# Performance work log

Measured on AMD Instinct MI355X. Metric: run time of the kernel, lower is better.

Reference implementation:

```python
import jax, jax.numpy as jnp
import numpy as np

DIM = 1024

def setup_inputs() -> dict:
    key = jax.random.key(0)
    ks = jax.random.split(key, 6)
    B, T, D = 8, 2048, DIM
    s = 1.0 / np.sqrt(D)
    x = jax.random.normal(ks[0], (B, T, D), dtype=jnp.float32)
    Wq = jax.random.normal(ks[1], (D, D), dtype=jnp.float32) * s
    Wk = jax.random.normal(ks[2], (D, D), dtype=jnp.float32) * s
    Wv = jax.random.normal(ks[3], (D, D), dtype=jnp.float32) * s
    Wp = jax.random.normal(ks[4], (D, D), dtype=jnp.float32) * s
    bp = jax.random.normal(ks[5], (D,), dtype=jnp.float32) * 0.01
    return {"x": x, "Wq": Wq, "Wk": Wk, "Wv": Wv, "Wp": Wp, "bp": bp}

def reference(x, Wq, Wk, Wv, Wp, bp):
    # x: [b, t, d]; weights stored as [d_in, d_out] (torch Linear applies x @ W.T;
    # here we bake the transpose into the stored matrix).
    scale = x.shape[-1] ** (-0.5)
    q = jnp.einsum('btd,de->bte', x, Wq)
    k = jnp.einsum('btd,de->bte', x, Wk)
    v = jnp.einsum('btd,de->bte', x, Wv)
    attn = jax.nn.softmax(jnp.einsum('btd,bTd->btT', q, k) * scale, axis=-1)
    out = jnp.einsum('btT,bTd->btd', attn, v)
    return jnp.einsum('btd,de->bte', out, Wp) + bp
```

## Files before the change

kernel.cpp:

```cpp
#include <hip/hip_runtime.h>


typedef _Float16 half_t;
typedef _Float16 half8 __attribute__((ext_vector_type(8)));
typedef float floatx4 __attribute__((ext_vector_type(4)));

#define GLD16(gp, lp)                                                          \
    __builtin_amdgcn_global_load_lds(                                          \
        (const __attribute__((address_space(1))) void*)(gp),                   \
        (__attribute__((address_space(3))) void*)(lp), 16, 0, 0)

#define WAIT_VM0()  asm volatile("s_waitcnt vmcnt(0)" ::: "memory")
#define BARRIER()   do { asm volatile("" ::: "memory");                        \
                         __builtin_amdgcn_s_barrier();                         \
                         asm volatile("" ::: "memory"); } while (0)

template<int EPI>
__global__ __launch_bounds__(512, 4)
void gemm16(const half_t* __restrict__ A, const half_t* __restrict__ B,
            void* __restrict__ Cv, void* __restrict__ C2, void* __restrict__ C3,
            const float* __restrict__ bias, int K, int lda, int ldb, int ldc,
            long long bsA, long long bsB, long long bsC)
{
    __shared__ half_t As[2 * 256 * 32];
    __shared__ half_t Bs[2 * 128 * 32];

    const int tid  = threadIdx.x;
    const int lane = tid & 63;
    const int wid  = tid >> 6;
    const int wr   = (wid >> 1) * 64;
    const int wc   = (wid & 1) * 64;
    const long long z = blockIdx.z;
    const int rowBase = blockIdx.y * 256;
    const int colBase = blockIdx.x * 128;

    const int lrow = lane >> 2;
    const int scol = (((lane & 3) ^ ((lane >> 3) & 3))) * 8;

    const half_t* gptr[3];
    int  lofs[3];
    bool isA[3];
    #pragma unroll
    for (int j = 0; j < 3; ++j) {
        const int r16 = (wid * 3 + j) * 16;
        if (r16 < 256) {
            gptr[j] = A + z * bsA + (long long)(rowBase + r16 + lrow) * lda + scol;
            lofs[j] = r16 * 32;
            isA[j]  = true;
        } else {
            gptr[j] = B + z * bsB + (long long)(colBase + (r16 - 256) + lrow) * ldb + scol;
            lofs[j] = (r16 - 256) * 32;
            isA[j]  = false;
        }
    }

    floatx4 acc[4][4];
    #pragma unroll
    for (int m = 0; m < 4; ++m)
        #pragma unroll
        for (int n = 0; n < 4; ++n)
            #pragma unroll
            for (int j = 0; j < 4; ++j) acc[m][n][j] = 0.0f;

    const int fr  = lane & 15;
    const int fks = (((lane >> 4) ^ ((lane >> 1) & 3))) * 8;
    const int nIter = K >> 5;

    #pragma unroll
    for (int j = 0; j < 3; ++j)
        GLD16(gptr[j], isA[j] ? &As[lofs[j]] : &Bs[lofs[j]]);
    WAIT_VM0();
    BARRIER();

    for (int it = 0; it < nIter; ++it) {
        const int ca = (it & 1) * 8192;
        const int cb = (it & 1) * 4096;
        const int na = 8192 - ca;
        const int nb = 4096 - cb;
        if (it + 1 < nIter) {
            const int kk = (it + 1) << 5;
            #pragma unroll
            for (int j = 0; j < 3; ++j)
                GLD16(gptr[j] + kk, isA[j] ? &As[na + lofs[j]] : &Bs[nb + lofs[j]]);
        }

        half8 af[4], bf[4];
        #pragma unroll
        for (int m = 0; m < 4; ++m)
            af[m] = *(const half8*)&As[ca + (wr + m * 16 + fr) * 32 + fks];
        #pragma unroll
        for (int n = 0; n < 4; ++n)
            bf[n] = *(const half8*)&Bs[cb + (wc + n * 16 + fr) * 32 + fks];
        #pragma unroll
        for (int m = 0; m < 4; ++m)
            #pragma unroll
            for (int n = 0; n < 4; ++n)
                acc[m][n] = __builtin_amdgcn_mfma_f32_16x16x32_f16(af[m], bf[n], acc[m][n], 0, 0, 0);

        WAIT_VM0();
        BARRIER();
    }

    const int ecol = lane & 15;
    const int q4   = (lane >> 4) * 4;
    #pragma unroll
    for (int m = 0; m < 4; ++m) {
        #pragma unroll
        for (int n = 0; n < 4; ++n) {
            const int gcol = colBase + wc + n * 16 + ecol;
            #pragma unroll
            for (int r = 0; r < 4; ++r) {
                const int grow = rowBase + wr + m * 16 + q4 + r;
                float v = acc[m][n][r];
                if (EPI == 0) {
                    ((half_t*)Cv)[z * bsC + (long long)grow * ldc + gcol] = (half_t)v;
                } else if (EPI == 1) {
                    ((float*)Cv)[(long long)grow * ldc + gcol] = v + bias[gcol];
                } else {
                    const int mat = colBase >> 10;
                    const int c   = gcol & 1023;
                    if (mat == 0) {
                        ((half_t*)Cv)[(long long)grow * 1024 + c] = (half_t)(v * 0.03125f);
                    } else if (mat == 1) {
                        ((half_t*)C2)[(long long)grow * 1024 + c] = (half_t)v;
                    } else {
                        const long long bb = grow >> 11;
                        const long long tt = grow & 2047;
                        ((half_t*)C3)[bb * (1024LL * 2048) + (long long)c * 2048 + tt] = (half_t)v;
                    }
                }
            }
        }
    }
}

__global__ __launch_bounds__(256)
void cast16(const float* __restrict__ x, half_t* __restrict__ y)
{
    const long long i = ((long long)blockIdx.x * 256 + threadIdx.x) * 8;
    floatx4 a = *(const floatx4*)(x + i);
    floatx4 b = *(const floatx4*)(x + i + 4);
    half8 h;
    #pragma unroll
    for (int j = 0; j < 4; ++j) { h[j] = (half_t)a[j]; h[j + 4] = (half_t)b[j]; }
    *(half8*)(y + i) = h;
}

__global__ __launch_bounds__(256)
void cast_transpose4(const float* __restrict__ W0, const float* __restrict__ W1,
                     const float* __restrict__ W2, const float* __restrict__ W3,
                     half_t* __restrict__ WT)
{
    const float* W = (blockIdx.z == 0) ? W0 : (blockIdx.z == 1) ? W1
                   : (blockIdx.z == 2) ? W2 : W3;
    half_t* O = WT + (long long)blockIdx.z * 1024 * 1024;
    __shared__ float t[32][33];
    const int bx = blockIdx.x * 32, by = blockIdx.y * 32;
    const int tx = threadIdx.x, ty = threadIdx.y;
    #pragma unroll
    for (int i = 0; i < 32; i += 8)
        t[ty + i][tx] = W[(long long)(by + ty + i) * 1024 + bx + tx];
    __syncthreads();
    #pragma unroll
    for (int i = 0; i < 32; i += 8)
        O[(long long)(bx + ty + i) * 1024 + by + tx] = (half_t)t[tx][ty + i];
}

__global__ __launch_bounds__(256)
void softmax_rows(half_t* __restrict__ S)
{
    const long long base = (long long)blockIdx.x * 2048;
    const int t = threadIdx.x;
    half8 h = *(const half8*)(S + base + t * 8);
    float v[8];
    #pragma unroll
    for (int i = 0; i < 8; ++i) v[i] = (float)h[i];
    float m = -3.0e38f;
    #pragma unroll
    for (int i = 0; i < 8; ++i) m = fmaxf(m, v[i]);
    #pragma unroll
    for (int off = 32; off > 0; off >>= 1) m = fmaxf(m, __shfl_down(m, off));
    __shared__ float redm[4], reds[4];
    const int lane = t & 63, wid = t >> 6;
    if (lane == 0) redm[wid] = m;
    __syncthreads();
    const float M = fmaxf(fmaxf(redm[0], redm[1]), fmaxf(redm[2], redm[3]));
    float s = 0.f;
    #pragma unroll
    for (int i = 0; i < 8; ++i) { v[i] = __expf(v[i] - M); s += v[i]; }
    #pragma unroll
    for (int off = 32; off > 0; off >>= 1) s += __shfl_down(s, off);
    if (lane == 0) reds[wid] = s;
    __syncthreads();
    const float inv = 1.0f / (reds[0] + reds[1] + reds[2] + reds[3]);
    #pragma unroll
    for (int i = 0; i < 8; ++i) h[i] = (half_t)(v[i] * inv);
    *(half8*)(S + base + t * 8) = h;
}

extern "C" void kernel_launch(void* const* d_in, const int* in_sizes, int n_in,
                              void* d_out, int out_size, void* d_ws, size_t ws_size,
                              hipStream_t stream)
{
    const float* x  = (const float*)d_in[0];
    const float* Wq = (const float*)d_in[1];
    const float* Wk = (const float*)d_in[2];
    const float* Wv = (const float*)d_in[3];
    const float* Wp = (const float*)d_in[4];
    const float* bp = (const float*)d_in[5];
    float* out = (float*)d_out;

    char* ws = (char*)d_ws;
    const long long MB = 1024LL * 1024LL;
    half_t* WqkvT = (half_t*)(ws + 0 * MB);
    half_t* WpT   = (half_t*)(ws + 6 * MB);
    half_t* q     = (half_t*)(ws + 8 * MB);
    half_t* k     = (half_t*)(ws + 40 * MB);
    half_t* vT    = (half_t*)(ws + 72 * MB);
    half_t* x16   = (half_t*)(ws + 104 * MB);
    half_t* S     = (half_t*)(ws + 104 * MB);

    dim3 blk(512);
    cast16<<<8192, dim3(256), 0, stream>>>(x, x16);
    cast_transpose4<<<dim3(32, 32, 4), dim3(32, 8), 0, stream>>>(Wq, Wk, Wv, Wp, WqkvT);

    gemm16<2><<<dim3(24, 64, 1), blk, 0, stream>>>(
        x16, WqkvT, q, k, vT, nullptr, 1024, 1024, 1024, 0, 0, 0, 0);

    gemm16<0><<<dim3(16, 8, 8), blk, 0, stream>>>(
        q, k, S, nullptr, nullptr, nullptr, 1024, 1024, 1024, 2048,
        2048LL * 1024, 2048LL * 1024, 2048LL * 2048);

    softmax_rows<<<8 * 2048, dim3(256), 0, stream>>>(S);

    gemm16<0><<<dim3(8, 8, 8), blk, 0, stream>>>(
        S, vT, q, nullptr, nullptr, nullptr, 2048, 2048, 2048, 1024,
        2048LL * 2048, 1024LL * 2048, 2048LL * 1024);

    gemm16<1><<<dim3(8, 64, 1), blk, 0, stream>>>(
        q, WpT, out, nullptr, nullptr, bp, 1024, 1024, 1024, 1024, 0, 0, 0);
}
```

Measured before the change: 542.7 us.

## Rework GEMM to 256x256x64 tiles with phased LDS loads and XCD-aware block remap

Raises the GEMM block tile from 256x128x32 to 256x256x64, with each of 8 waves computing a 128x64 sub-tile. Loads are staged in phases with lgkmcnt waits, barriers and s_setprio around the MFMA bursts. It also remaps block IDs so neighbouring tiles land on the same XCD, which should improve L2 reuse. The aim is higher arithmetic intensity per LDS/global byte and fewer K-loop iterations, at the cost of more registers (launch bounds drop to 2 blocks per CU), more LDS, and half as many blocks in each launch.

```diff
diff --git a/kernel.cpp b/kernel.cpp
--- a/kernel.cpp
+++ b/kernel.cpp
@@ -10,107 +10,156 @@
         (const __attribute__((address_space(1))) void*)(gp),                   \
         (__attribute__((address_space(3))) void*)(lp), 16, 0, 0)
 
-#define WAIT_VM0()  asm volatile("s_waitcnt vmcnt(0)" ::: "memory")
+#define WAIT_VM0()   asm volatile("s_waitcnt vmcnt(0)" ::: "memory")
+#define WAIT_LGKM0() asm volatile("s_waitcnt lgkmcnt(0)" ::: "memory")
+#define WAIT_LGKM8() asm volatile("s_waitcnt lgkmcnt(8)" ::: "memory")
 #define BARRIER()   do { asm volatile("" ::: "memory");                        \
                          __builtin_amdgcn_s_barrier();                         \
                          asm volatile("" ::: "memory"); } while (0)
 
 template<int EPI>
-__global__ __launch_bounds__(512, 4)
+__global__ __launch_bounds__(512, 2)
 void gemm16(const half_t* __restrict__ A, const half_t* __restrict__ B,
             void* __restrict__ Cv, void* __restrict__ C2, void* __restrict__ C3,
             const float* __restrict__ bias, int K, int lda, int ldb, int ldc,
             long long bsA, long long bsB, long long bsC)
 {
-    __shared__ half_t As[2 * 256 * 32];
-    __shared__ half_t Bs[2 * 128 * 32];
+    __shared__ half_t As[2 * 2 * 128 * 64];
+    __shared__ half_t Bs[2 * 2 * 128 * 64];
 
     const int tid  = threadIdx.x;
     const int lane = tid & 63;
-    const int wid  = tid >> 6;
-    const int wr   = (wid >> 1) * 64;
-    const int wc   = (wid & 1) * 64;
-    const long long z = blockIdx.z;
-    const int rowBase = blockIdx.y * 256;
-    const int colBase = blockIdx.x * 128;
-
-    const int lrow = lane >> 2;
-    const int scol = (((lane & 3) ^ ((lane >> 3) & 3))) * 8;
-
-    const half_t* gptr[3];
-    int  lofs[3];
-    bool isA[3];
-    #pragma unroll
-    for (int j = 0; j < 3; ++j) {
-        const int r16 = (wid * 3 + j) * 16;
-        if (r16 < 256) {
-            gptr[j] = A + z * bsA + (long long)(rowBase + r16 + lrow) * lda + scol;
-            lofs[j] = r16 * 32;
-            isA[j]  = true;
-        } else {
-            gptr[j] = B + z * bsB + (long long)(colBase + (r16 - 256) + lrow) * ldb + scol;
-            lofs[j] = (r16 - 256) * 32;
-            isA[j]  = false;
-        }
-    }
-
-    floatx4 acc[4][4];
-    #pragma unroll
-    for (int m = 0; m < 4; ++m)
+    const int w    = tid >> 6;
+    const int wm   = w >> 2;
+    const int wn   = w & 3;
+
+    int bx = blockIdx.x, by = blockIdx.y, bz = blockIdx.z;
+    {
+        const int gx = gridDim.x, gy = gridDim.y;
+        const int nwg = gx * gy * (int)gridDim.z;
+        int lid = (bz * gy + by) * gx + bx;
+        const int qq = nwg >> 3, rr = nwg & 7;
+        const int xcd = lid & 7, off = lid >> 3;
+        lid = (xcd < rr ? xcd * (qq + 1) : rr * (qq + 1) + (xcd - rr) * qq) + off;
+        bx = lid % gx; lid /= gx;
+        by = lid % gy; bz = lid / gy;
+    }
+    const long long z = bz;
+    const int rowBase = by * 256;
+    const int colBase = bx * 256;
+
+    const int srow = lane >> 3;
+    const int schk = (lane & 7) ^ srow;
+    const half_t* gp[4];
+    int jstep[4];
+    half_t* lp[4];
+    #pragma unroll
+    for (int i = 0; i < 4; ++i) {
+        const bool ia = (i < 2);
+        const int ld  = ia ? lda : ldb;
+        const int rb  = (ia ? rowBase : colBase) + (i & 1) * 128 + w * 16 + srow;
+        gp[i] = (ia ? A + z * bsA : B + z * bsB) + (long long)rb * ld + schk * 8;
+        jstep[i] = 8 * ld;
+        lp[i] = (ia ? As : Bs) + (i & 1) * 8192 + w * 1024;
+    }
+
+    const int fr  = lane & 15;
+    const int q   = lane >> 4;
+    const int rsw = fr & 7;
+    const half_t* Abase = As + wm * 8192 + fr * 64;
+    const half_t* Bbase = Bs + (wn >> 1) * 8192 + ((wn & 1) * 64 + fr) * 64;
+    const int ko0 = ((0 + q) ^ rsw) * 8;
+    const int ko1 = ((4 + q) ^ rsw) * 8;
+
+    floatx4 acc[8][4];
+    #pragma unroll
+    for (int m = 0; m < 8; ++m)
         #pragma unroll
         for (int n = 0; n < 4; ++n)
             #pragma unroll
             for (int j = 0; j < 4; ++j) acc[m][n][j] = 0.0f;
 
-    const int fr  = lane & 15;
-    const int fks = (((lane >> 4) ^ ((lane >> 1) & 3))) * 8;
-    const int nIter = K >> 5;
-
-    #pragma unroll
-    for (int j = 0; j < 3; ++j)
-        GLD16(gptr[j], isA[j] ? &As[lofs[j]] : &Bs[lofs[j]]);
+    const int nIter = K >> 6;
+
+    #pragma unroll
+    for (int i = 0; i < 4; ++i) {
+        GLD16(gp[i],            lp[i]);
+        GLD16(gp[i] + jstep[i], lp[i] + 512);
+    }
     WAIT_VM0();
     BARRIER();
 
-    for (int it = 0; it < nIter; ++it) {
-        const int ca = (it & 1) * 8192;
-        const int cb = (it & 1) * 4096;
-        const int na = 8192 - ca;
-        const int nb = 4096 - cb;
-        if (it + 1 < nIter) {
-            const int kk = (it + 1) << 5;
-            #pragma unroll
-            for (int j = 0; j < 3; ++j)
-                GLD16(gptr[j] + kk, isA[j] ? &As[na + lofs[j]] : &Bs[nb + lofs[j]]);
-        }
-
-        half8 af[4], bf[4];
-        #pragma unroll
-        for (int m = 0; m < 4; ++m)
-            af[m] = *(const half8*)&As[ca + (wr + m * 16 + fr) * 32 + fks];
-        #pragma unroll
-        for (int n = 0; n < 4; ++n)
-            bf[n] = *(const half8*)&Bs[cb + (wc + n * 16 + fr) * 32 + fks];
-        #pragma unroll
-        for (int m = 0; m < 4; ++m)
+    for (int t = 0; t < nIter; ++t) {
+        const int cbuf = (t & 1) << 14;
+        const int nbuf = 16384 - cbuf;
+        half8 bf[4][2], af[2][2];
+
+        if (t + 1 < nIter) {
+            const int kk = (t + 1) << 6;
+            #pragma unroll
+            for (int i = 0; i < 4; ++i) {
+                GLD16(gp[i] + kk,            lp[i] + nbuf);
+                GLD16(gp[i] + kk + jstep[i], lp[i] + nbuf + 512);
+            }
+        }
+        #pragma unroll
+        for (int n = 0; n < 4; ++n) {
+            bf[n][0] = *(const half8*)(Bbase + cbuf + n * 1024 + ko0);
+            bf[n][1] = *(const half8*)(Bbase + cbuf + n * 1024 + ko1);
+        }
+        af[0][0] = *(const half8*)(Abase + cbuf + 0 * 1024 + ko0);
+        af[0][1] = *(const half8*)(Abase + cbuf + 0 * 1024 + ko1);
+        af[1][0] = *(const half8*)(Abase + cbuf + 1 * 1024 + ko0);
+        af[1][1] = *(const half8*)(Abase + cbuf + 1 * 1024 + ko1);
+        WAIT_LGKM8();
+        BARRIER();
+        WAIT_LGKM0();
+        __builtin_amdgcn_s_setprio(1);
+        #pragma unroll
+        for (int ml = 0; ml < 2; ++ml)
             #pragma unroll
             for (int n = 0; n < 4; ++n)
-                acc[m][n] = __builtin_amdgcn_mfma_f32_16x16x32_f16(af[m], bf[n], acc[m][n], 0, 0, 0);
-
-        WAIT_VM0();
+                #pragma unroll
+                for (int ks = 0; ks < 2; ++ks)
+                    acc[ml][n] = __builtin_amdgcn_mfma_f32_16x16x32_f16(
+                        af[ml][ks], bf[n][ks], acc[ml][n], 0, 0, 0);
+        __builtin_amdgcn_s_setprio(0);
         BARRIER();
+
+        #pragma unroll
+        for (int p = 1; p < 4; ++p) {
+            #pragma unroll
+            for (int ml = 0; ml < 2; ++ml) {
+                af[ml][0] = *(const half8*)(Abase + cbuf + (p * 2 + ml) * 1024 + ko0);
+                af[ml][1] = *(const half8*)(Abase + cbuf + (p * 2 + ml) * 1024 + ko1);
+            }
+            BARRIER();
+            WAIT_LGKM0();
+            __builtin_amdgcn_s_setprio(1);
+            #pragma unroll
+            for (int ml = 0; ml < 2; ++ml)
+                #pragma unroll
+                for (int n = 0; n < 4; ++n)
+                    #pragma unroll
+                    for (int ks = 0; ks < 2; ++ks)
+                        acc[p * 2 + ml][n] = __builtin_amdgcn_mfma_f32_16x16x32_f16(
+                            af[ml][ks], bf[n][ks], acc[p * 2 + ml][n], 0, 0, 0);
+            __builtin_amdgcn_s_setprio(0);
+            if (p == 3) WAIT_VM0();
+            BARRIER();
+        }
     }
 
     const int ecol = lane & 15;
     const int q4   = (lane >> 4) * 4;
     #pragma unroll
-    for (int m = 0; m < 4; ++m) {
+    for (int m = 0; m < 8; ++m) {
         #pragma unroll
         for (int n = 0; n < 4; ++n) {
-            const int gcol = colBase + wc + n * 16 + ecol;
+            const int gcol = colBase + wn * 64 + n * 16 + ecol;
             #pragma unroll
             for (int r = 0; r < 4; ++r) {
-                const int grow = rowBase + wr + m * 16 + q4 + r;
+                const int grow = rowBase + wm * 128 + m * 16 + q4 + r;
                 float v = acc[m][n][r];
                 if (EPI == 0) {
                     ((half_t*)Cv)[z * bsC + (long long)grow * ldc + gcol] = (half_t)v;
@@ -224,19 +273,19 @@
     cast16<<<8192, dim3(256), 0, stream>>>(x, x16);
     cast_transpose4<<<dim3(32, 32, 4), dim3(32, 8), 0, stream>>>(Wq, Wk, Wv, Wp, WqkvT);
 
-    gemm16<2><<<dim3(24, 64, 1), blk, 0, stream>>>(
+    gemm16<2><<<dim3(12, 64, 1), blk, 0, stream>>>(
         x16, WqkvT, q, k, vT, nullptr, 1024, 1024, 1024, 0, 0, 0, 0);
 
-    gemm16<0><<<dim3(16, 8, 8), blk, 0, stream>>>(
+    gemm16<0><<<dim3(8, 8, 8), blk, 0, stream>>>(
         q, k, S, nullptr, nullptr, nullptr, 1024, 1024, 1024, 2048,
         2048LL * 1024, 2048LL * 1024, 2048LL * 2048);
 
     softmax_rows<<<8 * 2048, dim3(256), 0, stream>>>(S);
 
-    gemm16<0><<<dim3(8, 8, 8), blk, 0, stream>>>(
+    gemm16<0><<<dim3(4, 8, 8), blk, 0, stream>>>(
         S, vT, q, nullptr, nullptr, nullptr, 2048, 2048, 2048, 1024,
         2048LL * 2048, 1024LL * 2048, 2048LL * 1024);
 
-    gemm16<1><<<dim3(8, 64, 1), blk, 0, stream>>>(
+    gemm16<1><<<dim3(4, 64, 1), blk, 0, stream>>>(
         q, WpT, out, nullptr, nullptr, bp, 1024, 1024, 1024, 1024, 0, 0, 0);
 }
```

New measurement: 538.9 us. About the same (-0.7%).

## Shrink GEMM tile to 128x128 with 256 threads and add XCD-aware block remap

Applied to the files above, without the earlier changes.

Reduces the GEMM block tile from 256x128 (8 waves) to 128x128 (4 waves), halving LDS use per block and doubling grid size for all four GEMM launches. It also remaps linear workgroup IDs so that consecutive tiles land on the same XCD, aiming for better L2 locality on the chiplet design. The smaller tile lowers per-block data reuse (more global/L2 traffic per FLOP) in exchange for higher occupancy and better load balance.

```diff
diff --git a/kernel.cpp b/kernel.cpp
--- a/kernel.cpp
+++ b/kernel.cpp
@@ -16,40 +16,52 @@
                          asm volatile("" ::: "memory"); } while (0)
 
 template<int EPI>
-__global__ __launch_bounds__(512, 4)
+__global__ __launch_bounds__(256, 4)
 void gemm16(const half_t* __restrict__ A, const half_t* __restrict__ B,
             void* __restrict__ Cv, void* __restrict__ C2, void* __restrict__ C3,
             const float* __restrict__ bias, int K, int lda, int ldb, int ldc,
             long long bsA, long long bsB, long long bsC)
 {
-    __shared__ half_t As[2 * 256 * 32];
+    __shared__ half_t As[2 * 128 * 32];
     __shared__ half_t Bs[2 * 128 * 32];
 
     const int tid  = threadIdx.x;
     const int lane = tid & 63;
-    const int wid  = tid >> 6;
-    const int wr   = (wid >> 1) * 64;
-    const int wc   = (wid & 1) * 64;
-    const long long z = blockIdx.z;
-    const int rowBase = blockIdx.y * 256;
-    const int colBase = blockIdx.x * 128;
+    const int w    = tid >> 6;
+    const int wm   = w >> 1;
+    const int wn   = w & 1;
+
+    int bx = blockIdx.x, by = blockIdx.y, bz = blockIdx.z;
+    {
+        const int gx = gridDim.x, gy = gridDim.y;
+        const int nwg = gx * gy * (int)gridDim.z;
+        int lid = (bz * gy + by) * gx + bx;
+        const int qq = nwg >> 3, rr = nwg & 7;
+        const int xcd = lid & 7, off = lid >> 3;
+        lid = (xcd < rr ? xcd * (qq + 1) : rr * (qq + 1) + (xcd - rr) * qq) + off;
+        bx = lid % gx; lid /= gx;
+        by = lid % gy; bz = lid / gy;
+    }
+    const long long z = bz;
+    const int rowBase = by * 128;
+    const int colBase = bx * 128;
 
     const int lrow = lane >> 2;
     const int scol = (((lane & 3) ^ ((lane >> 3) & 3))) * 8;
 
-    const half_t* gptr[3];
-    int  lofs[3];
-    bool isA[3];
-    #pragma unroll
-    for (int j = 0; j < 3; ++j) {
-        const int r16 = (wid * 3 + j) * 16;
-        if (r16 < 256) {
-            gptr[j] = A + z * bsA + (long long)(rowBase + r16 + lrow) * lda + scol;
-            lofs[j] = r16 * 32;
+    const half_t* gptr[4];
+    int  lofs[4];
+    bool isA[4];
+    #pragma unroll
+    for (int j = 0; j < 4; ++j) {
+        const int g = w * 4 + j;
+        if (g < 8) {
+            gptr[j] = A + z * bsA + (long long)(rowBase + g * 16 + lrow) * lda + scol;
+            lofs[j] = g * 16 * 32;
             isA[j]  = true;
         } else {
-            gptr[j] = B + z * bsB + (long long)(colBase + (r16 - 256) + lrow) * ldb + scol;
-            lofs[j] = (r16 - 256) * 32;
+            gptr[j] = B + z * bsB + (long long)(colBase + (g - 8) * 16 + lrow) * ldb + scol;
+            lofs[j] = (g - 8) * 16 * 32;
             isA[j]  = false;
         }
     }
@@ -67,30 +79,28 @@
     const int nIter = K >> 5;
 
     #pragma unroll
-    for (int j = 0; j < 3; ++j)
+    for (int j = 0; j < 4; ++j)
         GLD16(gptr[j], isA[j] ? &As[lofs[j]] : &Bs[lofs[j]]);
     WAIT_VM0();
     BARRIER();
 
     for (int it = 0; it < nIter; ++it) {
-        const int ca = (it & 1) * 8192;
-        const int cb = (it & 1) * 4096;
-        const int na = 8192 - ca;
-        const int nb = 4096 - cb;
+        const int cur = (it & 1) * 4096;
+        const int nxt = 4096 - cur;
         if (it + 1 < nIter) {
             const int kk = (it + 1) << 5;
             #pragma unroll
-            for (int j = 0; j < 3; ++j)
-                GLD16(gptr[j] + kk, isA[j] ? &As[na + lofs[j]] : &Bs[nb + lofs[j]]);
+            for (int j = 0; j < 4; ++j)
+                GLD16(gptr[j] + kk, isA[j] ? &As[nxt + lofs[j]] : &Bs[nxt + lofs[j]]);
         }
 
         half8 af[4], bf[4];
         #pragma unroll
         for (int m = 0; m < 4; ++m)
-            af[m] = *(const half8*)&As[ca + (wr + m * 16 + fr) * 32 + fks];
+            af[m] = *(const half8*)&As[cur + (wm * 64 + m * 16 + fr) * 32 + fks];
         #pragma unroll
         for (int n = 0; n < 4; ++n)
-            bf[n] = *(const half8*)&Bs[cb + (wc + n * 16 + fr) * 32 + fks];
+            bf[n] = *(const half8*)&Bs[cur + (wn * 64 + n * 16 + fr) * 32 + fks];
         #pragma unroll
         for (int m = 0; m < 4; ++m)
             #pragma unroll
@@ -107,10 +117,10 @@
     for (int m = 0; m < 4; ++m) {
         #pragma unroll
         for (int n = 0; n < 4; ++n) {
-            const int gcol = colBase + wc + n * 16 + ecol;
+            const int gcol = colBase + wn * 64 + n * 16 + ecol;
             #pragma unroll
             for (int r = 0; r < 4; ++r) {
-                const int grow = rowBase + wr + m * 16 + q4 + r;
+                const int grow = rowBase + wm * 64 + m * 16 + q4 + r;
                 float v = acc[m][n][r];
                 if (EPI == 0) {
                     ((half_t*)Cv)[z * bsC + (long long)grow * ldc + gcol] = (half_t)v;
@@ -220,23 +230,23 @@
     half_t* x16   = (half_t*)(ws + 104 * MB);
     half_t* S     = (half_t*)(ws + 104 * MB);
 
-    dim3 blk(512);
+    dim3 blk(256);
     cast16<<<8192, dim3(256), 0, stream>>>(x, x16);
     cast_transpose4<<<dim3(32, 32, 4), dim3(32, 8), 0, stream>>>(Wq, Wk, Wv, Wp, WqkvT);
 
-    gemm16<2><<<dim3(24, 64, 1), blk, 0, stream>>>(
+    gemm16<2><<<dim3(24, 128, 1), blk, 0, stream>>>(
         x16, WqkvT, q, k, vT, nullptr, 1024, 1024, 1024, 0, 0, 0, 0);
 
-    gemm16<0><<<dim3(16, 8, 8), blk, 0, stream>>>(
+    gemm16<0><<<dim3(16, 16, 8), blk, 0, stream>>>(
         q, k, S, nullptr, nullptr, nullptr, 1024, 1024, 1024, 2048,
         2048LL * 1024, 2048LL * 1024, 2048LL * 2048);
 
     softmax_rows<<<8 * 2048, dim3(256), 0, stream>>>(S);
 
-    gemm16<0><<<dim3(8, 8, 8), blk, 0, stream>>>(
+    gemm16<0><<<dim3(8, 16, 8), blk, 0, stream>>>(
         S, vT, q, nullptr, nullptr, nullptr, 2048, 2048, 2048, 1024,
         2048LL * 2048, 1024LL * 2048, 2048LL * 1024);
 
-    gemm16<1><<<dim3(8, 64, 1), blk, 0, stream>>>(
+    gemm16<1><<<dim3(8, 128, 1), blk, 0, stream>>>(
         q, WpT, out, nullptr, nullptr, bp, 1024, 1024, 1024, 1024, 0, 0, 0);
 }
```

After: 514.5 us. 5.2% less time.
